# Optimization experiments

Measured on AMD Instinct MI355X. Metric: run time of the kernel, lower is better.

Reference implementation:

```python
import jax, jax.numpy as jnp
import numpy as np

B, TV, TS, D = 16, 256, 32, 512


def setup_inputs() -> dict:
    key = jax.random.key(0)
    ks = jax.random.split(key, 8)
    return {
        "video_feature": jax.random.normal(ks[0], (B, TV, D), dtype=jnp.float32),
        "video_mask": jnp.ones((B, TV), dtype=jnp.float32),
        "sentence_feature": jax.random.normal(ks[1], (B, TS, D), dtype=jnp.float32),
        "sentence_mask": jnp.ones((B, TS), dtype=jnp.float32),
        "w1": jax.random.normal(ks[2], (D, D), dtype=jnp.float32) * (1.0 / np.sqrt(D)),
        "b1": jax.random.normal(ks[3], (D,), dtype=jnp.float32) * 0.02,
        "w2": jax.random.normal(ks[4], (D, D), dtype=jnp.float32) * (1.0 / np.sqrt(D)),
        "wt": jax.random.normal(ks[5], (D,), dtype=jnp.float32) * (1.0 / np.sqrt(D)),
    }


def reference(video_feature, video_mask, sentence_feature, sentence_mask, w1, b1, w2, wt):
    # tmp1: [B, Tv, D] masked video projection (Linear with bias)
    tmp1 = (jnp.einsum("bvd,ed->bve", video_feature, w1) + b1) * video_mask[:, :, None]
    # tmp2: [B, Ts, D] masked sentence projection (Linear, no bias)
    tmp2 = jnp.einsum("bsd,ed->bse", sentence_feature, w2) * sentence_mask[:, :, None]
    # pairwise mask: [B, Tv, Ts]
    pair_mask = video_mask[:, :, None] * sentence_mask[:, None, :]
    # broadcast-add -> [B, Tv, Ts, D], mask, tanh, reduce with wt -> [B, Tv, Ts]
    tmp = (tmp1[:, :, None, :] + tmp2[:, None, :, :]) * pair_mask[..., None]
    M = jnp.einsum("bvsd,d->bvs", jnp.tanh(tmp), wt)
    return M * pair_mask
```

## Files before the change

### kernel.cpp

```cpp
#include <hip/hip_runtime.h>

#define BB 16
#define TV 256
#define TS 32
#define DD 512

typedef float    floatx4  __attribute__((ext_vector_type(4)));
typedef short    short8   __attribute__((ext_vector_type(8)));
typedef unsigned short ushort8 __attribute__((ext_vector_type(8)));

static __device__ __forceinline__ unsigned short f2bf(float f) {
    unsigned int u = __float_as_uint(f);
    u += 0x7FFFu + ((u >> 16) & 1u);
    return (unsigned short)(u >> 16);
}

__global__ __launch_bounds__(256) void ta_convert(
    const float* __restrict__ video, const float* __restrict__ sent,
    const float* __restrict__ w1,    const float* __restrict__ w2,
    unsigned short* __restrict__ vb, unsigned short* __restrict__ sb,
    unsigned short* __restrict__ w1b, unsigned short* __restrict__ w2b)
{
    const int NV = BB * TV * DD, NS = BB * TS * DD, NW = DD * DD;
    const int base = (blockIdx.x * 256 + threadIdx.x) * 8;
    const float* src; unsigned short* dst; int off;
    if      (base < NV)           { src = video; dst = vb;  off = base; }
    else if (base < NV + NS)      { src = sent;  dst = sb;  off = base - NV; }
    else if (base < NV + NS + NW) { src = w1;    dst = w1b; off = base - NV - NS; }
    else                          { src = w2;    dst = w2b; off = base - NV - NS - NW; }
    const float4 a = *(const float4*)(src + off);
    const float4 b = *(const float4*)(src + off + 4);
    ushort8 o;
    o[0] = f2bf(a.x); o[1] = f2bf(a.y); o[2] = f2bf(a.z); o[3] = f2bf(a.w);
    o[4] = f2bf(b.x); o[5] = f2bf(b.y); o[6] = f2bf(b.z); o[7] = f2bf(b.w);
    *(ushort8*)(dst + off) = o;
}

__global__ __launch_bounds__(256) void ta_mfma_gemm(
    const unsigned short* __restrict__ vb, const unsigned short* __restrict__ w1b,
    const float* __restrict__ b1,          const float* __restrict__ vmask,
    unsigned short* __restrict__ tmp1,
    const unsigned short* __restrict__ sb, const unsigned short* __restrict__ w2b,
    const float* __restrict__ smask,       unsigned short* __restrict__ tmp2,
    const float* __restrict__ wt,          float* __restrict__ wsum)
{
    const int t = threadIdx.x;

    if (blockIdx.x == 0 && t < 64) {
        float v = 0.f;
        for (int i = t; i < DD; i += 64) v += wt[i];
        for (int off = 32; off; off >>= 1) v += __shfl_down(v, off);
        if (t == 0) wsum[0] = v;
    }

    const bool g2 = (blockIdx.x >= 512);
    const int bid = g2 ? (int)blockIdx.x - 512 : (int)blockIdx.x;
    const unsigned short* __restrict__ A = g2 ? sb    : vb;
    const unsigned short* __restrict__ W = g2 ? w2b   : w1b;
    const float* __restrict__ rm         = g2 ? smask : vmask;
    const int m0 = (g2 ? (bid & 7)  : (bid & 63)) * 64;
    const int n0 = (g2 ? (bid >> 3) : (bid >> 6)) * 64;

    __shared__ unsigned short As[2][4096];
    __shared__ unsigned short Bs[2][4096];

    const int lane = t & 63;
    const int wid  = t >> 6;
    const int wm   = wid >> 1, wn = wid & 1;
    const int lr   = lane & 15, kg = lane >> 4;

    const int r0 = t >> 3,          g0c = (t & 7) ^ (r0 & 7);
    const int r1 = (t + 256) >> 3,  g1c = (t & 7) ^ (r1 & 7);
    const unsigned short* a0p = A + (size_t)(m0 + r0) * DD + g0c * 8;
    const unsigned short* a1p = A + (size_t)(m0 + r1) * DD + g1c * 8;
    const unsigned short* w0p = W + (size_t)(n0 + r0) * DD + g0c * 8;
    const unsigned short* w1p = W + (size_t)(n0 + r1) * DD + g1c * 8;
    const int l0 = t * 8;
    const int l1 = (t + 256) * 8;

#define TA_STAGE(buf, koff) do {                                               \
    __builtin_amdgcn_global_load_lds(                                          \
        (const __attribute__((address_space(1))) void*)(a0p + (koff)),         \
        (__attribute__((address_space(3))) void*)&As[buf][l0], 16, 0, 0);      \
    __builtin_amdgcn_global_load_lds(                                          \
        (const __attribute__((address_space(1))) void*)(a1p + (koff)),         \
        (__attribute__((address_space(3))) void*)&As[buf][l1], 16, 0, 0);      \
    __builtin_amdgcn_global_load_lds(                                          \
        (const __attribute__((address_space(1))) void*)(w0p + (koff)),         \
        (__attribute__((address_space(3))) void*)&Bs[buf][l0], 16, 0, 0);      \
    __builtin_amdgcn_global_load_lds(                                          \
        (const __attribute__((address_space(1))) void*)(w1p + (koff)),         \
        (__attribute__((address_space(3))) void*)&Bs[buf][l1], 16, 0, 0);      \
  } while (0)

    floatx4 acc[2][2] = {};

    const int ml0 = wm * 32 + lr, ml1 = ml0 + 16;
    const int nl0 = wn * 32 + lr, nl1 = nl0 + 16;
    const int sa0 = ml0 * 64, sa1 = ml1 * 64;
    const int sb0 = nl0 * 64, sb1 = nl1 * 64;
    const int xa = ml0 & 7, xb = nl0 & 7;

    TA_STAGE(0, 0);
    __syncthreads();

    int cur = 0;
    for (int step = 0; step < 8; ++step) {
        if (step < 7) TA_STAGE(cur ^ 1, (step + 1) * 64);
#pragma unroll
        for (int kk = 0; kk < 2; ++kk) {
            const int kc = kk * 4 + kg;
            short8 a0 = *(const short8*)&As[cur][sa0 + ((kc ^ xa) << 3)];
            short8 a1 = *(const short8*)&As[cur][sa1 + ((kc ^ xa) << 3)];
            short8 b0 = *(const short8*)&Bs[cur][sb0 + ((kc ^ xb) << 3)];
            short8 b1 = *(const short8*)&Bs[cur][sb1 + ((kc ^ xb) << 3)];
            acc[0][0] = __builtin_amdgcn_mfma_f32_16x16x32_bf16(a0, b0, acc[0][0], 0, 0, 0);
            acc[0][1] = __builtin_amdgcn_mfma_f32_16x16x32_bf16(a0, b1, acc[0][1], 0, 0, 0);
            acc[1][0] = __builtin_amdgcn_mfma_f32_16x16x32_bf16(a1, b0, acc[1][0], 0, 0, 0);
            acc[1][1] = __builtin_amdgcn_mfma_f32_16x16x32_bf16(a1, b1, acc[1][1], 0, 0, 0);
        }
        __syncthreads();
        cur ^= 1;
    }
#undef TA_STAGE

#pragma unroll
    for (int fm = 0; fm < 2; ++fm)
#pragma unroll
        for (int fn = 0; fn < 2; ++fn)
#pragma unroll
            for (int r = 0; r < 4; ++r) {
                const int m = m0 + wm * 32 + fm * 16 + kg * 4 + r;
                const int n = n0 + wn * 32 + fn * 16 + lr;
                const float mk = rm[m];
                const float val = acc[fm][fn][r];
                if (!g2) tmp1[(size_t)m * DD + n] = f2bf((val + b1[n]) * mk);
                else     tmp2[(size_t)m * DD + n] = f2bf(val * mk);
            }
}

__global__ __launch_bounds__(512) void ta_tanh_main(
    const unsigned short* __restrict__ tmp1,
    const unsigned short* __restrict__ tmp2,
    const float* __restrict__ wt,
    const float* __restrict__ wsum,
    const float* __restrict__ vmask,
    const float* __restrict__ smask,
    float* __restrict__ out)
{
    __shared__ unsigned short t2s[TS * DD];
    __shared__ float part[512];

    const int t  = threadIdx.x;
    const int b  = blockIdx.x >> 6;
    const int v0 = (blockIdx.x & 63) << 2;

    {
        const unsigned short* src = tmp2 + (size_t)b * TS * DD;
#pragma unroll
        for (int i = 0; i < 4; ++i) {
            const int chunk = t + 512 * i;
            const int row = chunk >> 6;
            const int c   = chunk & 63;
            ushort8 val = *(const ushort8*)&src[chunk * 8];
            *(ushort8*)&t2s[row * DD + ((c ^ (row & 15)) << 3)] = val;
        }
    }
    __syncthreads();

    const int s  = t & 31;
    const int vi = (t >> 5) & 3;
    const int q  = __builtin_amdgcn_readfirstlane(t >> 7);
    const int v  = v0 + vi;

    const float pm = vmask[b * TV + v] * smask[b * TS + s];
    const float ce = pm * 2.885390082f;
    const unsigned short* __restrict__ x1p = tmp1 + ((size_t)(b * TV + v)) * DD + q * 128;
    const float* __restrict__ wtp = wt + q * 128;
    const int rowbase = s * DD;
    const int swz = s & 15;

    float acc0 = 0.f, acc1 = 0.f;
    for (int i = 0; i < 16; ++i) {
        ushort8 x2v = *(const ushort8*)&t2s[rowbase + (((q * 16 + i) ^ swz) << 3)];
        ushort8 x1v = *(const ushort8*)&x1p[i * 8];
#pragma unroll
        for (int j = 0; j < 4; ++j) {
            const float x1f = __uint_as_float((unsigned)x1v[j] << 16);
            const float x2f = __uint_as_float((unsigned)x2v[j] << 16);
            const float e   = __builtin_amdgcn_exp2f((x1f + x2f) * ce);
            acc0 = fmaf(wtp[i * 8 + j], __builtin_amdgcn_rcpf(e + 1.f), acc0);
        }
#pragma unroll
        for (int j = 4; j < 8; ++j) {
            const float x1f = __uint_as_float((unsigned)x1v[j] << 16);
            const float x2f = __uint_as_float((unsigned)x2v[j] << 16);
            const float e   = __builtin_amdgcn_exp2f((x1f + x2f) * ce);
            acc1 = fmaf(wtp[i * 8 + j], __builtin_amdgcn_rcpf(e + 1.f), acc1);
        }
    }

    part[t] = acc0 + acc1;
    __syncthreads();

    if (t < 128) {
        const float sum = part[t] + part[t + 128] + part[t + 256] + part[t + 384];
        const int s2 = t & 31, vi2 = t >> 5;
        const int v2 = v0 + vi2;
        const float pm2 = vmask[b * TV + v2] * smask[b * TS + s2];
        out[((size_t)b * TV + v2) * TS + s2] = pm2 * (wsum[0] - 2.f * sum);
    }
}

extern "C" void kernel_launch(void* const* d_in, const int* in_sizes, int n_in,
                              void* d_out, int out_size, void* d_ws, size_t ws_size,
                              hipStream_t stream)
{
    const float* video = (const float*)d_in[0];
    const float* vmask = (const float*)d_in[1];
    const float* sent  = (const float*)d_in[2];
    const float* smask = (const float*)d_in[3];
    const float* w1    = (const float*)d_in[4];
    const float* b1    = (const float*)d_in[5];
    const float* w2    = (const float*)d_in[6];
    const float* wt    = (const float*)d_in[7];
    float* out = (float*)d_out;

    const size_t NV = (size_t)BB * TV * DD, NS = (size_t)BB * TS * DD, NW = (size_t)DD * DD;

    unsigned short* tmp1 = (unsigned short*)d_ws;
    unsigned short* tmp2 = tmp1 + NV;
    unsigned short* vb   = tmp2 + NS;
    unsigned short* sb   = vb + NV;
    unsigned short* w1b  = sb + NS;
    unsigned short* w2b  = w1b + NW;
    float* wsum          = (float*)(w2b + NW);

    const int total8 = (int)((NV + NS + 2 * NW) / 8);
    ta_convert<<<dim3(total8 / 256), dim3(256), 0, stream>>>(
        video, sent, w1, w2, vb, sb, w1b, w2b);
    ta_mfma_gemm<<<dim3(512 + 64), dim3(256), 0, stream>>>(
        vb, w1b, b1, vmask, tmp1, sb, w2b, smask, tmp2, wt, wsum);
    ta_tanh_main<<<dim3(BB * (TV / 4)), dim3(512), 0, stream>>>(
        tmp1, tmp2, wt, wsum, vmask, smask, out);
}
```

Measured before the change: 41.91 us.

## Fuse video projection GEMM into tanh kernel using factored exp form

Moves the video projection GEMM into the tanh-reduce kernel so the tmp1 intermediate never round-trips through global memory. Each block computes a 16-row slice of tmp1 with MFMA, streaming the W1 tiles through LDS. The tanh is rewritten as exp(x1+x2) = exp(x1)*exp(x2), with both exponentials precomputed once, so the inner loop per element needs only an FMA and a reciprocal instead of an exp. The trade-offs are clamping plus bf16 rounding of the exponentials, which costs accuracy. Only 256 blocks run, and each one reloads all of W1, so the GEMM is redundant per batch and parallelism is lower.

```diff
diff --git a/kernel.cpp b/kernel.cpp
--- a/kernel.cpp
+++ b/kernel.cpp
@@ -9,20 +9,35 @@
 typedef short    short8   __attribute__((ext_vector_type(8)));
 typedef unsigned short ushort8 __attribute__((ext_vector_type(8)));
 
+#define TANH_SCALE 2.885390082f
+
 static __device__ __forceinline__ unsigned short f2bf(float f) {
     unsigned int u = __float_as_uint(f);
     u += 0x7FFFu + ((u >> 16) & 1u);
     return (unsigned short)(u >> 16);
 }
 
+#define GLL(srcp, dstp)                                                        \
+    __builtin_amdgcn_global_load_lds(                                          \
+        (const __attribute__((address_space(1))) void*)(srcp),                 \
+        (__attribute__((address_space(3))) void*)(dstp), 16, 0, 0)
+
 __global__ __launch_bounds__(256) void ta_convert(
     const float* __restrict__ video, const float* __restrict__ sent,
     const float* __restrict__ w1,    const float* __restrict__ w2,
     unsigned short* __restrict__ vb, unsigned short* __restrict__ sb,
-    unsigned short* __restrict__ w1b, unsigned short* __restrict__ w2b)
+    unsigned short* __restrict__ w1b, unsigned short* __restrict__ w2b,
+    const float* __restrict__ wt,    float* __restrict__ wsum)
 {
     const int NV = BB * TV * DD, NS = BB * TS * DD, NW = DD * DD;
-    const int base = (blockIdx.x * 256 + threadIdx.x) * 8;
+    const int t = threadIdx.x;
+    if (blockIdx.x == 0 && t < 64) {
+        float v = 0.f;
+        for (int i = t; i < DD; i += 64) v += wt[i];
+        for (int off = 32; off; off >>= 1) v += __shfl_down(v, off);
+        if (t == 0) wsum[0] = v;
+    }
+    const int base = (blockIdx.x * 256 + t) * 8;
     const float* src; unsigned short* dst; int off;
     if      (base < NV)           { src = video; dst = vb;  off = base; }
     else if (base < NV + NS)      { src = sent;  dst = sb;  off = base - NV; }
@@ -36,30 +51,14 @@
     *(ushort8*)(dst + off) = o;
 }
 
-__global__ __launch_bounds__(256) void ta_mfma_gemm(
-    const unsigned short* __restrict__ vb, const unsigned short* __restrict__ w1b,
-    const float* __restrict__ b1,          const float* __restrict__ vmask,
-    unsigned short* __restrict__ tmp1,
+__global__ __launch_bounds__(256) void ta_g2(
     const unsigned short* __restrict__ sb, const unsigned short* __restrict__ w2b,
-    const float* __restrict__ smask,       unsigned short* __restrict__ tmp2,
-    const float* __restrict__ wt,          float* __restrict__ wsum)
+    const float* __restrict__ smask,       unsigned short* __restrict__ tmp2e)
 {
     const int t = threadIdx.x;
-
-    if (blockIdx.x == 0 && t < 64) {
-        float v = 0.f;
-        for (int i = t; i < DD; i += 64) v += wt[i];
-        for (int off = 32; off; off >>= 1) v += __shfl_down(v, off);
-        if (t == 0) wsum[0] = v;
-    }
-
-    const bool g2 = (blockIdx.x >= 512);
-    const int bid = g2 ? (int)blockIdx.x - 512 : (int)blockIdx.x;
-    const unsigned short* __restrict__ A = g2 ? sb    : vb;
-    const unsigned short* __restrict__ W = g2 ? w2b   : w1b;
-    const float* __restrict__ rm         = g2 ? smask : vmask;
-    const int m0 = (g2 ? (bid & 7)  : (bid & 63)) * 64;
-    const int n0 = (g2 ? (bid >> 3) : (bid >> 6)) * 64;
+    const int bid = blockIdx.x;
+    const int m0 = (bid & 7) * 64;
+    const int n0 = (bid >> 3) * 64;
 
     __shared__ unsigned short As[2][4096];
     __shared__ unsigned short Bs[2][4096];
@@ -71,42 +70,29 @@
 
     const int r0 = t >> 3,          g0c = (t & 7) ^ (r0 & 7);
     const int r1 = (t + 256) >> 3,  g1c = (t & 7) ^ (r1 & 7);
-    const unsigned short* a0p = A + (size_t)(m0 + r0) * DD + g0c * 8;
-    const unsigned short* a1p = A + (size_t)(m0 + r1) * DD + g1c * 8;
-    const unsigned short* w0p = W + (size_t)(n0 + r0) * DD + g0c * 8;
-    const unsigned short* w1p = W + (size_t)(n0 + r1) * DD + g1c * 8;
-    const int l0 = t * 8;
-    const int l1 = (t + 256) * 8;
-
-#define TA_STAGE(buf, koff) do {                                               \
-    __builtin_amdgcn_global_load_lds(                                          \
-        (const __attribute__((address_space(1))) void*)(a0p + (koff)),         \
-        (__attribute__((address_space(3))) void*)&As[buf][l0], 16, 0, 0);      \
-    __builtin_amdgcn_global_load_lds(                                          \
-        (const __attribute__((address_space(1))) void*)(a1p + (koff)),         \
-        (__attribute__((address_space(3))) void*)&As[buf][l1], 16, 0, 0);      \
-    __builtin_amdgcn_global_load_lds(                                          \
-        (const __attribute__((address_space(1))) void*)(w0p + (koff)),         \
-        (__attribute__((address_space(3))) void*)&Bs[buf][l0], 16, 0, 0);      \
-    __builtin_amdgcn_global_load_lds(                                          \
-        (const __attribute__((address_space(1))) void*)(w1p + (koff)),         \
-        (__attribute__((address_space(3))) void*)&Bs[buf][l1], 16, 0, 0);      \
+    const unsigned short* a0p = sb  + (size_t)(m0 + r0) * DD + g0c * 8;
+    const unsigned short* a1p = sb  + (size_t)(m0 + r1) * DD + g1c * 8;
+    const unsigned short* w0p = w2b + (size_t)(n0 + r0) * DD + g0c * 8;
+    const unsigned short* w1p = w2b + (size_t)(n0 + r1) * DD + g1c * 8;
+    const int l0 = t * 8, l1 = (t + 256) * 8;
+
+#define G2_STAGE(buf, koff) do {                                               \
+    GLL(a0p + (koff), &As[buf][l0]); GLL(a1p + (koff), &As[buf][l1]);          \
+    GLL(w0p + (koff), &Bs[buf][l0]); GLL(w1p + (koff), &Bs[buf][l1]);          \
   } while (0)
 
     floatx4 acc[2][2] = {};
-
     const int ml0 = wm * 32 + lr, ml1 = ml0 + 16;
     const int nl0 = wn * 32 + lr, nl1 = nl0 + 16;
     const int sa0 = ml0 * 64, sa1 = ml1 * 64;
     const int sb0 = nl0 * 64, sb1 = nl1 * 64;
     const int xa = ml0 & 7, xb = nl0 & 7;
 
-    TA_STAGE(0, 0);
+    G2_STAGE(0, 0);
     __syncthreads();
-
     int cur = 0;
     for (int step = 0; step < 8; ++step) {
-        if (step < 7) TA_STAGE(cur ^ 1, (step + 1) * 64);
+        if (step < 7) G2_STAGE(cur ^ 1, (step + 1) * 64);
 #pragma unroll
         for (int kk = 0; kk < 2; ++kk) {
             const int kc = kk * 4 + kg;
@@ -122,7 +108,7 @@
         __syncthreads();
         cur ^= 1;
     }
-#undef TA_STAGE
+#undef G2_STAGE
 
 #pragma unroll
     for (int fm = 0; fm < 2; ++fm)
@@ -132,84 +118,126 @@
             for (int r = 0; r < 4; ++r) {
                 const int m = m0 + wm * 32 + fm * 16 + kg * 4 + r;
                 const int n = n0 + wn * 32 + fn * 16 + lr;
-                const float mk = rm[m];
-                const float val = acc[fm][fn][r];
-                if (!g2) tmp1[(size_t)m * DD + n] = f2bf((val + b1[n]) * mk);
-                else     tmp2[(size_t)m * DD + n] = f2bf(val * mk);
+                float z = acc[fm][fn][r] * smask[m] * TANH_SCALE;
+                z = fminf(fmaxf(z, -30.f), 30.f);
+                tmp2e[(size_t)m * DD + n] = f2bf(__builtin_amdgcn_exp2f(z));
             }
 }
 
-__global__ __launch_bounds__(512) void ta_tanh_main(
-    const unsigned short* __restrict__ tmp1,
-    const unsigned short* __restrict__ tmp2,
-    const float* __restrict__ wt,
-    const float* __restrict__ wsum,
-    const float* __restrict__ vmask,
-    const float* __restrict__ smask,
+__global__ __launch_bounds__(256, 2) void ta_fused(
+    const unsigned short* __restrict__ vb, const unsigned short* __restrict__ w1b,
+    const float* __restrict__ b1,          const float* __restrict__ vmask,
+    const float* __restrict__ smask,       const unsigned short* __restrict__ tmp2e,
+    const float* __restrict__ wt,          const float* __restrict__ wsum,
     float* __restrict__ out)
 {
-    __shared__ unsigned short t2s[TS * DD];
-    __shared__ float part[512];
-
-    const int t  = threadIdx.x;
-    const int b  = blockIdx.x >> 6;
-    const int v0 = (blockIdx.x & 63) << 2;
-
+    __shared__ unsigned short As[16 * 512];
+    __shared__ unsigned short Bs[2][64 * 64];
+    __shared__ unsigned short E1[16 * 512];
+    __shared__ unsigned short E2[32 * 512];
+
+    const int t   = threadIdx.x;
+    const int bid = blockIdx.x;
+    const int b   = bid >> 4;
+    const int v0  = (bid & 15) << 4;
+
+#pragma unroll
+    for (int i = 0; i < 4; ++i) {
+        const int c = t + 256 * i;
+        const int row = c >> 6, sc = (c & 63) ^ (row & 7);
+        GLL(vb + (size_t)(b * TV + v0 + row) * DD + sc * 8, &As[c * 8]);
+    }
+#pragma unroll
+    for (int i = 0; i < 8; ++i) {
+        const int c = t + 256 * i;
+        const int row = c >> 6, sc = (c & 63) ^ (row & 7);
+        GLL(tmp2e + (size_t)(b * TS + row) * DD + sc * 8, &E2[c * 8]);
+    }
     {
-        const unsigned short* src = tmp2 + (size_t)b * TS * DD;
-#pragma unroll
-        for (int i = 0; i < 4; ++i) {
-            const int chunk = t + 512 * i;
-            const int row = chunk >> 6;
-            const int c   = chunk & 63;
-            ushort8 val = *(const ushort8*)&src[chunk * 8];
-            *(ushort8*)&t2s[row * DD + ((c ^ (row & 15)) << 3)] = val;
-        }
+        const int c0 = t,       br0 = c0 >> 3, w0c = (c0 & 7) ^ (br0 & 7);
+        const int c1 = t + 256, br1 = c1 >> 3, w1c = (c1 & 7) ^ (br1 & 7);
+        GLL(w1b + (size_t)br0 * DD + w0c * 8, &Bs[0][c0 * 8]);
+        GLL(w1b + (size_t)br1 * DD + w1c * 8, &Bs[0][c1 * 8]);
     }
     __syncthreads();
 
-    const int s  = t & 31;
-    const int vi = (t >> 5) & 3;
-    const int q  = __builtin_amdgcn_readfirstlane(t >> 7);
-    const int v  = v0 + vi;
-
-    const float pm = vmask[b * TV + v] * smask[b * TS + s];
-    const float ce = pm * 2.885390082f;
-    const unsigned short* __restrict__ x1p = tmp1 + ((size_t)(b * TV + v)) * DD + q * 128;
-    const float* __restrict__ wtp = wt + q * 128;
-    const int rowbase = s * DD;
-    const int swz = s & 15;
-
-    float acc0 = 0.f, acc1 = 0.f;
-    for (int i = 0; i < 16; ++i) {
-        ushort8 x2v = *(const ushort8*)&t2s[rowbase + (((q * 16 + i) ^ swz) << 3)];
-        ushort8 x1v = *(const ushort8*)&x1p[i * 8];
-#pragma unroll
-        for (int j = 0; j < 4; ++j) {
-            const float x1f = __uint_as_float((unsigned)x1v[j] << 16);
-            const float x2f = __uint_as_float((unsigned)x2v[j] << 16);
-            const float e   = __builtin_amdgcn_exp2f((x1f + x2f) * ce);
-            acc0 = fmaf(wtp[i * 8 + j], __builtin_amdgcn_rcpf(e + 1.f), acc0);
-        }
-#pragma unroll
-        for (int j = 4; j < 8; ++j) {
-            const float x1f = __uint_as_float((unsigned)x1v[j] << 16);
-            const float x2f = __uint_as_float((unsigned)x2v[j] << 16);
-            const float e   = __builtin_amdgcn_exp2f((x1f + x2f) * ce);
-            acc1 = fmaf(wtp[i * 8 + j], __builtin_amdgcn_rcpf(e + 1.f), acc1);
-        }
-    }
-
-    part[t] = acc0 + acc1;
-    __syncthreads();
-
-    if (t < 128) {
-        const float sum = part[t] + part[t + 128] + part[t + 256] + part[t + 384];
-        const int s2 = t & 31, vi2 = t >> 5;
-        const int v2 = v0 + vi2;
-        const float pm2 = vmask[b * TV + v2] * smask[b * TS + s2];
-        out[((size_t)b * TV + v2) * TS + s2] = pm2 * (wsum[0] - 2.f * sum);
-    }
+    const int lane = t & 63;
+    const int wid  = t >> 6;
+    const int lr   = lane & 15, kg = lane >> 4;
+    const int brow = wid * 16 + lr;
+    const int xb   = brow & 7, xa = lr & 7;
+    const int saB  = brow * 64;
+
+    floatx4 acc = {0.f, 0.f, 0.f, 0.f};
+    int cur = 0;
+    for (int it = 0; it < 64; ++it) {
+        if (it < 63) {
+            const int nit = it + 1;
+            const int nn0 = (nit >> 3) * 64, nk0 = (nit & 7) * 64;
+            const int c0 = t,       br0 = c0 >> 3, w0c = (c0 & 7) ^ (br0 & 7);
+            const int c1 = t + 256, br1 = c1 >> 3, w1c = (c1 & 7) ^ (br1 & 7);
+            GLL(w1b + (size_t)(nn0 + br0) * DD + nk0 + w0c * 8, &Bs[cur ^ 1][c0 * 8]);
+            GLL(w1b + (size_t)(nn0 + br1) * DD + nk0 + w1c * 8, &Bs[cur ^ 1][c1 * 8]);
+        }
+        const int kbase = (it & 7) * 64;
+#pragma unroll
+        for (int kk = 0; kk < 2; ++kk) {
+            const int kc = kk * 4 + kg;
+            short8 a = *(const short8*)&As[lr * DD + kbase + ((kc ^ xa) << 3)];
+            short8 bf = *(const short8*)&Bs[cur][saB + ((kc ^ xb) << 3)];
+            acc = __builtin_amdgcn_mfma_f32_16x16x32_bf16(a, bf, acc, 0, 0, 0);
+        }
+        if ((it & 7) == 7) {
+            const int n0 = (it >> 3) * 64;
+#pragma unroll
+            for (int r = 0; r < 4; ++r) {
+                const int m = kg * 4 + r;
+                const int n = n0 + wid * 16 + lr;
+                const float mk = vmask[b * TV + v0 + m] * TANH_SCALE;
+                float z = (acc[r] + b1[n]) * mk;
+                z = fminf(fmaxf(z, -30.f), 30.f);
+                const float e = __builtin_amdgcn_exp2f(z);
+                E1[m * DD + (((n >> 3) ^ (m & 7)) << 3) + (n & 7)] = f2bf(e);
+            }
+            acc = (floatx4){0.f, 0.f, 0.f, 0.f};
+        }
+        __syncthreads();
+        cur ^= 1;
+    }
+
+    const int s2 = t & 15;
+    const int v  = t >> 4;
+    const int xv = v & 7, xl = s2 & 7, xh = (s2 + 16) & 7;
+    const unsigned short* e1p = E1 + v * DD;
+    const unsigned short* e2l = E2 + s2 * DD;
+    const unsigned short* e2h = E2 + (s2 + 16) * DD;
+
+    float accL = 0.f, accH = 0.f;
+#pragma unroll 8
+    for (int c = 0; c < 64; ++c) {
+        ushort8 e1 = *(const ushort8*)&e1p[(c ^ xv) << 3];
+        ushort8 al = *(const ushort8*)&e2l[(c ^ xl) << 3];
+        ushort8 ah = *(const ushort8*)&e2h[(c ^ xh) << 3];
+        floatx4 wA = *(const floatx4*)(wt + c * 8);
+        floatx4 wB = *(const floatx4*)(wt + c * 8 + 4);
+#pragma unroll
+        for (int j = 0; j < 8; ++j) {
+            const float w  = (j < 4) ? wA[j] : wB[j - 4];
+            const float x1 = __uint_as_float((unsigned)e1[j] << 16);
+            const float yl = __uint_as_float((unsigned)al[j] << 16);
+            const float yh = __uint_as_float((unsigned)ah[j] << 16);
+            accL = fmaf(w, __builtin_amdgcn_rcpf(fmaf(x1, yl, 1.f)), accL);
+            accH = fmaf(w, __builtin_amdgcn_rcpf(fmaf(x1, yh, 1.f)), accH);
+        }
+    }
+
+    const float ws = wsum[0];
+    const float vm = vmask[b * TV + v0 + v];
+    const float pmL = vm * smask[b * TS + s2];
+    const float pmH = vm * smask[b * TS + s2 + 16];
+    float* orow = out + ((size_t)(b * TV + v0 + v)) * TS;
+    orow[s2]      = pmL * (ws - 2.f * accL);
+    orow[s2 + 16] = pmH * (ws - 2.f * accH);
 }
 
 extern "C" void kernel_launch(void* const* d_in, const int* in_sizes, int n_in,
@@ -228,19 +256,17 @@
 
     const size_t NV = (size_t)BB * TV * DD, NS = (size_t)BB * TS * DD, NW = (size_t)DD * DD;
 
-    unsigned short* tmp1 = (unsigned short*)d_ws;
-    unsigned short* tmp2 = tmp1 + NV;
-    unsigned short* vb   = tmp2 + NS;
-    unsigned short* sb   = vb + NV;
-    unsigned short* w1b  = sb + NS;
-    unsigned short* w2b  = w1b + NW;
-    float* wsum          = (float*)(w2b + NW);
+    unsigned short* tmp2e = (unsigned short*)d_ws;
+    unsigned short* vb    = tmp2e + NS;
+    unsigned short* sb    = vb + NV;
+    unsigned short* w1b   = sb + NS;
+    unsigned short* w2b   = w1b + NW;
+    float* wsum           = (float*)(w2b + NW);
 
     const int total8 = (int)((NV + NS + 2 * NW) / 8);
     ta_convert<<<dim3(total8 / 256), dim3(256), 0, stream>>>(
-        video, sent, w1, w2, vb, sb, w1b, w2b);
-    ta_mfma_gemm<<<dim3(512 + 64), dim3(256), 0, stream>>>(
-        vb, w1b, b1, vmask, tmp1, sb, w2b, smask, tmp2, wt, wsum);
-    ta_tanh_main<<<dim3(BB * (TV / 4)), dim3(512), 0, stream>>>(
-        tmp1, tmp2, wt, wsum, vmask, smask, out);
-}
+        video, sent, w1, w2, vb, sb, w1b, w2b, wt, wsum);
+    ta_g2<<<dim3(64), dim3(256), 0, stream>>>(sb, w2b, smask, tmp2e);
+    ta_fused<<<dim3(256), dim3(256), 0, stream>>>(
+        vb, w1b, b1, vmask, smask, tmp2e, wt, wsum, out);
+}
```

Result: slower. 63.21 us (+50.8%).
